# Optimization experiments

Hardware: AMD Instinct MI355X
Metric: run time of the kernel (lower is better)

Reference implementation:

```python
import jax, jax.numpy as jnp
import numpy as np

B, S, E, F = 8, 1024, 1024, 4096
EPS = 1e-12

def _layer_norm(x, gamma, beta):
    mu = jnp.mean(x, axis=-1, keepdims=True)
    var = jnp.mean(jnp.square(x - mu), axis=-1, keepdims=True)
    return (x - mu) / jnp.sqrt(var + EPS) * gamma + beta

def setup_inputs() -> dict:
    key = jax.random.key(0)
    ks = jax.random.split(key, 16)
    sE = 1.0 / np.sqrt(E)
    sF = 1.0 / np.sqrt(F)
    return {
        'hidden_states': jax.random.normal(ks[0], (B, S, E), jnp.float32),
        'Wq': jax.random.normal(ks[1], (E, E), jnp.float32) * sE,
        'bq': jnp.zeros((E,), jnp.float32),
        'Wk': jax.random.normal(ks[2], (E, E), jnp.float32) * sE,
        'bk': jnp.zeros((E,), jnp.float32),
        'Wv': jax.random.normal(ks[3], (E, E), jnp.float32) * sE,
        'bv': jnp.zeros((E,), jnp.float32),
        'Wd': jax.random.normal(ks[4], (E, E), jnp.float32) * sE,
        'bd': jnp.zeros((E,), jnp.float32),
        'g1': jnp.ones((E,), jnp.float32),
        'b1': jnp.zeros((E,), jnp.float32),
        'Wi': jax.random.normal(ks[5], (E, F), jnp.float32) * sE,
        'bi': jnp.zeros((F,), jnp.float32),
        'Wo': jax.random.normal(ks[6], (F, E), jnp.float32) * sF,
        'bo': jnp.zeros((E,), jnp.float32),
        'g2': jnp.ones((E,), jnp.float32),
        'b2': jnp.zeros((E,), jnp.float32),
    }

def reference(hidden_states, Wq, bq, Wk, bk, Wv, bv, Wd, bd, g1, b1, Wi, bi, Wo, bo, g2, b2):
    x = hidden_states
    q = x @ Wq + bq                     # [B,S,E]
    k = x @ Wk + bk
    v = x @ Wv + bv
    scores = jnp.einsum('bqe,bke->bqk', q, k) / jnp.sqrt(jnp.float32(E))
    attn_w = jax.nn.softmax(scores, axis=-1)
    attn_out = jnp.einsum('bqk,bke->bqe', attn_w, v)
    # add_norm 1 (dropout = identity in eval)
    h1 = _layer_norm(attn_out @ Wd + bd + x, g1, b1)
    ff = jax.nn.gelu(h1 @ Wi + bi, approximate=False)   # forward_act
    # NOTE: original code's second add_norm uses forward_act (pre out_dense),
    # applying out_dense inside add_norm -> LN(out_dense(ff) + h1)
    out = _layer_norm(ff @ Wo + bo + h1, g2, b2)
    return out
```

## Files before the change

kernel.cpp:

```cpp
#include <hip/hip_runtime.h>
#include <math.h>


typedef __bf16 bf16;
typedef __attribute__((ext_vector_type(8))) __bf16 bf16x8;
typedef __attribute__((ext_vector_type(4))) __bf16 bf16x4;
typedef __attribute__((ext_vector_type(4))) float f32x4;

#define BM 128
#define BN 128
#define BK 64
#define SCS 140

__device__ __forceinline__ void async_cp16(const bf16* g, bf16* l) {
    __builtin_amdgcn_global_load_lds((__attribute__((address_space(1))) void*)(g),
                                     (__attribute__((address_space(3))) void*)(l),
                                     16, 0, 0);
}

__device__ __forceinline__ float gelu_fast(float x) {
    float u = x * x;
    float y = 1.5957691216f * x * fmaf(0.044715f, u, 1.0f);
    float e = __expf(-y);
    return x * __builtin_amdgcn_rcpf(1.0f + e);
}

__device__ __forceinline__ float load_dual(const void* p, long long i, int f32) {
    return f32 ? ((const float*)p)[i] : (float)((const bf16*)p)[i];
}


__global__ void diag_init(const void* x, int* dflag)
{
    const int t = threadIdx.x;
    const bf16* xb = (const bf16*)x;
    float a = (float)xb[2 * t];
    float b = (float)xb[2 * t + 1];
    auto wild = [](float v) -> bool {
        float af = fabsf(v);
        return !(af <= 3.0e38f) || af > 1.0e3f || (v != 0.0f && af < 1.0e-8f);
    };
    unsigned long long ba = __ballot(wild(a));
    unsigned long long bb = __ballot(wild(b));
    if (t == 0) *dflag = (__popcll(ba) + __popcll(bb) > 16) ? 1 : 0;
}

__global__ void sentinel_small(float* out) { out[0] = 2048.0f; }


__global__ __launch_bounds__(256)
void convert_vec4(const void* src, bf16* dst, long long n4, const int* dflag)
{
    const int f32 = *dflag;
    long long i = (long long)blockIdx.x * 256 + threadIdx.x;
    if (i >= n4) return;
    bf16x4 o;
    if (f32) {
        f32x4 v = ((const f32x4*)src)[i];
        #pragma unroll
        for (int j = 0; j < 4; j++) o[j] = (bf16)v[j];
    } else {
        o = ((const bf16x4*)src)[i];
    }
    ((bf16x4*)dst)[i] = o;
}

struct SmallPtrs { const void* p[10]; };

__global__ __launch_bounds__(256)
void convert_small(SmallPtrs sp, bf16* dst, const int* dflag)
{
    const int f32 = *dflag;
    const int idx = blockIdx.x * 256 + threadIdx.x;
    if (idx >= 13312) return;
    const int seg = idx >> 10;
    float v;
    if (seg < 9) v = load_dual(sp.p[seg], idx & 1023, f32);
    else         v = load_dual(sp.p[9], idx - 9216, f32);
    dst[idx] = (bf16)v;
}

__global__ __launch_bounds__(256)
void transpose_dual(const void* in, bf16* out, int R, int C, const int* dflag)
{
    __shared__ bf16 tile[32][33];
    const int f32 = *dflag;
    const int c0 = blockIdx.x * 32, r0 = blockIdx.y * 32;
    const int tx = threadIdx.x, ty = threadIdx.y;
    #pragma unroll
    for (int i = 0; i < 32; i += 8)
        tile[ty + i][tx] = (bf16)load_dual(in, (long long)(r0 + ty + i) * C + (c0 + tx), f32);
    __syncthreads();
    #pragma unroll
    for (int i = 0; i < 32; i += 8)
        out[(long long)(c0 + ty + i) * R + (r0 + tx)] = tile[tx][ty + i];
}

__global__ __launch_bounds__(256)
void transpose_b(const bf16* __restrict__ in, bf16* __restrict__ out, int R, int C)
{
    __shared__ bf16 tile[32][33];
    const long long z = (long long)blockIdx.z * (long long)R * C;
    const int c0 = blockIdx.x * 32, r0 = blockIdx.y * 32;
    const int tx = threadIdx.x, ty = threadIdx.y;
    #pragma unroll
    for (int i = 0; i < 32; i += 8)
        tile[ty + i][tx] = in[z + (long long)(r0 + ty + i) * C + (c0 + tx)];
    __syncthreads();
    #pragma unroll
    for (int i = 0; i < 32; i += 8)
        out[z + (long long)(c0 + ty + i) * R + (r0 + tx)] = tile[tx][ty + i];
}

template<int ACT, int HAS_BIAS, int HAS_RES, int OUT_F32>
__global__ __launch_bounds__(512)
void gemm_bt(const bf16* __restrict__ A, const bf16* __restrict__ Bt,
             const bf16* __restrict__ bias, const bf16* __restrict__ res,
             void* __restrict__ Cout, int M, int N, int K, float scale,
             long long bsA, long long bsB, long long bsC, long long bsBias)
{
    __shared__ __align__(16) char smem[65536];
    float* sC = (float*)smem;

    const int tid  = threadIdx.x;
    const int lane = tid & 63;
    const int wave = tid >> 6;
    const int pw   = wave & 3;
    const int wm   = pw >> 1;
    const int wn   = pw & 1;
    const bool producer = (wave >= 4);
    const int m0   = blockIdx.y * BM;
    const int n0   = blockIdx.x * BN;
    const long long zA = (long long)blockIdx.z * bsA;
    const long long zB = (long long)blockIdx.z * bsB;
    const long long zC = (long long)blockIdx.z * bsC;
    const bf16* biasz = HAS_BIAS ? (bias + (long long)blockIdx.z * bsBias) : nullptr;
    const int nIter = K >> 6;

    f32x4 acc[4][4];
    const bf16* gA[4]; const bf16* gB[4]; int lo[4];

    if (producer) {
        #pragma unroll
        for (int j = 0; j < 4; j++) {
            const int ci  = j * 256 + pw * 64 + lane;
            const int row = ci >> 3;
            const int c8  = ((ci & 7) ^ (row & 7)) * 8;
            gA[j] = A + zA + (long long)(m0 + row) * K + c8;
            gB[j] = Bt + zB + (long long)(n0 + row) * K + c8;
            lo[j] = (j * 256 + pw * 64) * 8;
        }
        bf16* dA = (bf16*)smem;
        bf16* dB = (bf16*)(smem + 16384);
        #pragma unroll
        for (int j = 0; j < 4; j++) {
            async_cp16(gA[j], dA + lo[j]);
            async_cp16(gB[j], dB + lo[j]);
            gA[j] += BK; gB[j] += BK;
        }
    } else {
        const f32x4 zf = {0.f, 0.f, 0.f, 0.f};
        #pragma unroll
        for (int i = 0; i < 4; i++)
            #pragma unroll
            for (int j = 0; j < 4; j++) acc[i][j] = zf;
    }
    __syncthreads();

    const int fr   = lane & 15;
    const int x0   = (lane >> 4) ^ (fr & 7);
    const int arow = wm * 64 + fr;
    const int brow = wn * 64 + fr;

    for (int kt = 0; kt < nIter; ++kt) {
        if (producer) {
            if (kt + 1 < nIter) {
                const int bo = ((kt + 1) & 1) ? 32768 : 0;
                bf16* dA = (bf16*)(smem + bo);
                bf16* dB = (bf16*)(smem + bo + 16384);
                #pragma unroll
                for (int j = 0; j < 4; j++) {
                    async_cp16(gA[j], dA + lo[j]);
                    async_cp16(gB[j], dB + lo[j]);
                    gA[j] += BK; gB[j] += BK;
                }
            }
        } else {
            const int bo = (kt & 1) ? 32768 : 0;
            const bf16* sAk = (const bf16*)(smem + bo);
            const bf16* sBk = (const bf16*)(smem + bo + 16384);
            #pragma unroll
            for (int s = 0; s < 2; s++) {
                const int xo = (x0 ^ (s << 2)) * 8;
                bf16x8 afr[4], bfr[4];
                #pragma unroll
                for (int mi = 0; mi < 4; mi++) afr[mi] = *(const bf16x8*)(sAk + (arow + mi * 16) * 64 + xo);
                #pragma unroll
                for (int ni = 0; ni < 4; ni++) bfr[ni] = *(const bf16x8*)(sBk + (brow + ni * 16) * 64 + xo);
                #pragma unroll
                for (int mi = 0; mi < 4; mi++)
                    #pragma unroll
                    for (int ni = 0; ni < 4; ni++)
                        acc[mi][ni] = __builtin_amdgcn_mfma_f32_16x16x32_bf16(afr[mi], bfr[ni], acc[mi][ni], 0, 0, 0);
            }
        }
        __syncthreads();
    }

    const int q4 = lane >> 4;
    for (int h = 0; h < 2; h++) {
        __syncthreads();
        if (!producer && wm == h) {
            #pragma unroll
            for (int mi = 0; mi < 4; mi++)
                #pragma unroll
                for (int r = 0; r < 4; r++) {
                    const int lr = mi * 16 + q4 * 4 + r;
                    #pragma unroll
                    for (int ni = 0; ni < 4; ni++)
                        sC[lr * SCS + wn * 64 + ni * 16 + fr] = acc[mi][ni][r];
                }
        }
        __syncthreads();
        const int lr = tid >> 3;
        const int cb = (tid & 7) * 16;
        const long long grow  = m0 + h * 64 + lr;
        const long long gbase = zC + grow * (long long)N + (n0 + cb);
        const float* srow = sC + lr * SCS + cb;
        #pragma unroll
        for (int g = 0; g < 2; g++) {
            f32x4 v0 = *(const f32x4*)(srow + g * 8);
            f32x4 v1 = *(const f32x4*)(srow + g * 8 + 4);
            float vv[8] = {v0[0], v0[1], v0[2], v0[3], v1[0], v1[1], v1[2], v1[3]};
            if constexpr (HAS_BIAS) {
                bf16x8 bb = *(const bf16x8*)(biasz + n0 + cb + g * 8);
                #pragma unroll
                for (int j = 0; j < 8; j++) vv[j] = vv[j] * scale + (float)bb[j];
            } else {
                #pragma unroll
                for (int j = 0; j < 8; j++) vv[j] *= scale;
            }
            if constexpr (ACT == 1) {
                #pragma unroll
                for (int j = 0; j < 8; j++) vv[j] = gelu_fast(vv[j]);
            }
            if constexpr (HAS_RES) {
                bf16x8 rr = *(const bf16x8*)(res + gbase + g * 8);
                #pragma unroll
                for (int j = 0; j < 8; j++) vv[j] += (float)rr[j];
            }
            if constexpr (OUT_F32) {
                f32x4 o0 = {vv[0], vv[1], vv[2], vv[3]};
                f32x4 o1 = {vv[4], vv[5], vv[6], vv[7]};
                *(f32x4*)((float*)Cout + gbase + g * 8)     = o0;
                *(f32x4*)((float*)Cout + gbase + g * 8 + 4) = o1;
            } else {
                bf16x8 o;
                #pragma unroll
                for (int j = 0; j < 8; j++) o[j] = (bf16)vv[j];
                *(bf16x8*)((bf16*)Cout + gbase + g * 8) = o;
            }
        }
    }
}

template<int ACT, int HAS_BIAS, int HAS_RES, int OUT_F32, int SPLITK>
__global__ __launch_bounds__(512, 2)
void gemm256(const bf16* __restrict__ A, const bf16* __restrict__ Bt,
             const bf16* __restrict__ bias, const bf16* __restrict__ res,
             void* __restrict__ Cout, void* __restrict__ Cout2,
             int M, int N, int K, int ldk, float scale,
             long long bsB, long long bsC, long long bsBias)
{
    __shared__ __align__(16) char smem[131072];

    const int tid  = threadIdx.x;
    const int lane = tid & 63;
    const int wave = tid >> 6;
    const int wm   = wave >> 2;
    const int wn   = wave & 3;

    const int gx  = N >> 8;
    const int nwg = gx * (M >> 8);
    int wg = blockIdx.x;
    {
        const int q = nwg >> 3, r = nwg & 7;
        const int xcd = wg & 7, lid = wg >> 3;
        wg = (xcd < r ? xcd * (q + 1) : r * (q + 1) + (xcd - r) * q) + lid;
    }
    const int bx = wg % gx, by = wg / gx;
    const int m0 = by << 8, n0 = bx << 8;
    const int zi = blockIdx.y;

    const bf16* Ab = A  + (SPLITK ? (long long)zi * K : 0);
    const bf16* Bb = Bt + (SPLITK ? (long long)zi * K : (long long)zi * bsB);
    const bool  bon = HAS_BIAS && (!SPLITK || zi == 0);
    const bool  ron = HAS_RES  && (!SPLITK || zi == 0);
    const bf16* biasz = HAS_BIAS ? (bias + (SPLITK ? 0 : (long long)zi * bsBias)) : nullptr;
    const long long coff = SPLITK ? 0 : (long long)zi * bsC;
    char* const Cb = (char*)((SPLITK && zi) ? Cout2 : Cout);

    int soff[2];
    #pragma unroll
    for (int qq = 0; qq < 2; qq++) {
        const int g   = (wave * 2 + qq) * 64 + lane;
        const int rp  = g >> 3, sub = g & 7;
        const int row = rp * 2 + (sub >> 2);
        const int cc  = (sub & 3) ^ (rp & 3);
        soff[qq] = row * ldk + cc * 8;
    }
    const bf16* aS0 = Ab + (long long)m0 * ldk + soff[0];
    const bf16* aS1 = Ab + (long long)m0 * ldk + soff[1];
    const bf16* bS0 = Bb + (long long)n0 * ldk + soff[0];
    const bf16* bS1 = Bb + (long long)n0 * ldk + soff[1];
    char* const ldsW = smem + wave * 2048;

    const int fr = lane & 15, chk = lane >> 4;
    const int ra  = wm * 128 + fr;
    const int aRd = (ra >> 1) * 128 + (ra & 1) * 64 + ((chk ^ ((ra >> 1) & 3)) * 16);
    const int rb  = wn * 64 + fr;
    const int bRd = 32768 + (rb >> 1) * 128 + (rb & 1) * 64 + ((chk ^ ((rb >> 1) & 3)) * 16);

    unsigned aAddr[4], bAddr[4];
    {
        const unsigned sm3 = (unsigned)(size_t)(__attribute__((address_space(3))) char*)smem;
        #pragma unroll
        for (int cb = 0; cb < 2; cb++)
            #pragma unroll
            for (int s = 0; s < 2; s++) {
                aAddr[cb * 2 + s] = sm3 + cb * 65536 + s * 16384 + aRd;
                bAddr[cb * 2 + s] = sm3 + cb * 65536 + s * 16384 + bRd;
            }
    }

#define DSR(d, b, imm) \
    asm volatile("ds_read_b128 %0, %1 offset:%c2" : "=v"(d) : "v"(b), "i"(imm))

#define STG(buf, mat, h, t) do { \
    char* _d = ldsW + (buf) * 65536 + (mat) * 32768 + (h) * 16384; \
    const int _ko = (t) * 64 + (h) * 32; \
    async_cp16(((mat) ? bS0 : aS0) + _ko, (bf16*)_d); \
    async_cp16(((mat) ? bS1 : aS1) + _ko, (bf16*)(_d + 1024)); \
} while (0)
#define IF_STG(c, buf, mat, h, t) do { if (c) STG(buf, mat, h, t); } while (0)
#define NO_WAIT do {} while (0)
#define VM_WAIT(c) do { \
    if (c) asm volatile("s_waitcnt vmcnt(6)"); \
    else   asm volatile("s_waitcnt vmcnt(0)"); \
} while (0)
#define PHASE(cbuf, s, mh, DOB, STAGE_STMT, WAIT_STMT) do { \
    bf16x8 av0, av1, av2, av3; \
    DSR(av0, aAddr[(cbuf) * 2 + (s)], ((mh) * 4 + 0) * 1024); \
    DSR(av1, aAddr[(cbuf) * 2 + (s)], ((mh) * 4 + 1) * 1024); \
    DSR(av2, aAddr[(cbuf) * 2 + (s)], ((mh) * 4 + 2) * 1024); \
    DSR(av3, aAddr[(cbuf) * 2 + (s)], ((mh) * 4 + 3) * 1024); \
    if (DOB) { \
        DSR(bv[0], bAddr[(cbuf) * 2 + (s)], 0); \
        DSR(bv[1], bAddr[(cbuf) * 2 + (s)], 1024); \
        DSR(bv[2], bAddr[(cbuf) * 2 + (s)], 2048); \
        DSR(bv[3], bAddr[(cbuf) * 2 + (s)], 3072); \
    } \
    STAGE_STMT; \
    __builtin_amdgcn_s_barrier(); \
    asm volatile("s_waitcnt lgkmcnt(0)"); \
    __builtin_amdgcn_sched_barrier(0); \
    __builtin_amdgcn_s_setprio(1); \
    _Pragma("unroll") \
    for (int _j = 0; _j < 4; _j++) { \
        acc[(mh) * 4 + 0][_j] = __builtin_amdgcn_mfma_f32_16x16x32_bf16(av0, bv[_j], acc[(mh) * 4 + 0][_j], 0, 0, 0); \
        acc[(mh) * 4 + 1][_j] = __builtin_amdgcn_mfma_f32_16x16x32_bf16(av1, bv[_j], acc[(mh) * 4 + 1][_j], 0, 0, 0); \
        acc[(mh) * 4 + 2][_j] = __builtin_amdgcn_mfma_f32_16x16x32_bf16(av2, bv[_j], acc[(mh) * 4 + 2][_j], 0, 0, 0); \
        acc[(mh) * 4 + 3][_j] = __builtin_amdgcn_mfma_f32_16x16x32_bf16(av3, bv[_j], acc[(mh) * 4 + 3][_j], 0, 0, 0); \
    } \
    __builtin_amdgcn_s_setprio(0); \
    __builtin_amdgcn_sched_barrier(0); \
    WAIT_STMT; \
    __builtin_amdgcn_s_barrier(); \
} while (0)

    const int NT = K >> 6, NI = NT >> 1;

    STG(0, 1, 0, 0); STG(0, 0, 0, 0); STG(0, 1, 1, 0); STG(0, 0, 1, 0);
    STG(1, 1, 0, 1); STG(1, 0, 0, 1); STG(1, 1, 1, 1);

    f32x4 acc[8][4];
    {
        const f32x4 zf = {0.f, 0.f, 0.f, 0.f};
        #pragma unroll
        for (int i = 0; i < 8; i++)
            #pragma unroll
            for (int j = 0; j < 4; j++) acc[i][j] = zf;
    }
    bf16x8 bv[4];

    asm volatile("s_waitcnt vmcnt(6)");
    __builtin_amdgcn_s_barrier();

    for (int it = 0; it < NI; ++it) {
        const int o = 2 * it + 1, e2 = 2 * it + 2, o2 = 2 * it + 3;
        const bool se = e2 < NT, so = o2 < NT;
        PHASE(0, 0, 0, 1, STG(1, 0, 1, o),          NO_WAIT);
        PHASE(0, 0, 1, 0, IF_STG(se, 0, 1, 0, e2),  NO_WAIT);
        PHASE(0, 1, 0, 1, IF_STG(se, 0, 0, 0, e2),  NO_WAIT);
        PHASE(0, 1, 1, 0, IF_STG(se, 0, 1, 1, e2),  VM_WAIT(se));
        PHASE(1, 0, 0, 1, IF_STG(se, 0, 0, 1, e2),  NO_WAIT);
        PHASE(1, 0, 1, 0, IF_STG(so, 1, 1, 0, o2),  NO_WAIT);
        PHASE(1, 1, 0, 1, IF_STG(so, 1, 0, 0, o2),  NO_WAIT);
        PHASE(1, 1, 1, 0, IF_STG(so, 1, 1, 1, o2),  VM_WAIT(so));
    }
#undef PHASE
#undef VM_WAIT
#undef NO_WAIT
#undef IF_STG
#undef STG
#undef DSR

    float* sC = (float*)smem;
    const int q4 = lane >> 4;
    const int lr = tid >> 3;
    const int c0 = (tid & 7) * 4;
    const long long Nll = N;
    #pragma unroll
    for (int p = 0; p < 4; p++) {
        __syncthreads();
        if (wm == (p >> 1)) {
            #pragma unroll
            for (int i = 0; i < 4; i++) {
                const int fi = (p & 1) * 4 + i;
                #pragma unroll
                for (int r = 0; r < 4; r++) {
                    const int row = i * 16 + q4 * 4 + r;
                    #pragma unroll
                    for (int j = 0; j < 4; j++)
                        sC[row * 260 + wn * 64 + j * 16 + fr] = acc[fi][j][r];
                }
            }
        }
        __syncthreads();
        const long long grow = m0 + p * 64 + lr;
        const long long gb = grow * Nll + n0;
        const float* srow = sC + lr * 260;
        #pragma unroll
        for (int g = 0; g < 8; g++) {
            const int col = c0 + g * 32;
            f32x4 v = *(const f32x4*)(srow + col);
            float vv[4] = {v[0], v[1], v[2], v[3]};
            if (bon) {
                bf16x4 bb = *(const bf16x4*)(biasz + n0 + col);
                #pragma unroll
                for (int j = 0; j < 4; j++) vv[j] = vv[j] * scale + (float)bb[j];
            } else {
                #pragma unroll
                for (int j = 0; j < 4; j++) vv[j] *= scale;
            }
            if constexpr (ACT == 1) {
                #pragma unroll
                for (int j = 0; j < 4; j++) vv[j] = gelu_fast(vv[j]);
            }
            if (ron) {
                bf16x4 rr = *(const bf16x4*)(res + gb + col);
                #pragma unroll
                for (int j = 0; j < 4; j++) vv[j] += (float)rr[j];
            }
            if constexpr (OUT_F32) {
                f32x4 o4 = {vv[0], vv[1], vv[2], vv[3]};
                *(f32x4*)((float*)Cb + coff + gb + col) = o4;
            } else {
                bf16x4 o4;
                #pragma unroll
                for (int j = 0; j < 4; j++) o4[j] = (bf16)vv[j];
                *(bf16x4*)((bf16*)Cb + coff + gb + col) = o4;
            }
        }
    }
}


__global__ __launch_bounds__(256)
void softmax_inplace(bf16* __restrict__ P, int N)
{
    const long long row = blockIdx.x;
    bf16* p = P + row * (long long)N;
    const int t = threadIdx.x;
    bf16x4 xin = *(const bf16x4*)(p + t * 4);
    float xs[4];
    #pragma unroll
    for (int i = 0; i < 4; i++) xs[i] = (float)xin[i];

    float m = fmaxf(fmaxf(xs[0], xs[1]), fmaxf(xs[2], xs[3]));
    #pragma unroll
    for (int off = 32; off > 0; off >>= 1) m = fmaxf(m, __shfl_xor(m, off, 64));
    __shared__ float red[4];
    if ((t & 63) == 0) red[t >> 6] = m;
    __syncthreads();
    m = fmaxf(fmaxf(red[0], red[1]), fmaxf(red[2], red[3]));

    float e[4], s = 0.f;
    #pragma unroll
    for (int i = 0; i < 4; i++) { e[i] = __expf(xs[i] - m); s += e[i]; }
    #pragma unroll
    for (int off = 32; off > 0; off >>= 1) s += __shfl_xor(s, off, 64);
    __shared__ float red2[4];
    if ((t & 63) == 0) red2[t >> 6] = s;
    __syncthreads();
    s = red2[0] + red2[1] + red2[2] + red2[3];
    const float inv = 1.f / s;

    bf16x4 o;
    #pragma unroll
    for (int i = 0; i < 4; i++) o[i] = (bf16)(e[i] * inv);
    *(bf16x4*)(p + t * 4) = o;
}

template<int IN_MODE, int OUT_F32>
__global__ __launch_bounds__(256)
void layernorm_rows(const void* __restrict__ Z, const void* __restrict__ Z2,
                    const bf16* __restrict__ g, const bf16* __restrict__ b,
                    void* __restrict__ outp, int N)
{
    const long long row = blockIdx.x;
    const int t = threadIdx.x;
    float xv[4];
    if constexpr (IN_MODE >= 1) {
        f32x4 zin = *(const f32x4*)((const float*)Z + row * (long long)N + t * 4);
        #pragma unroll
        for (int i = 0; i < 4; i++) xv[i] = zin[i];
        if constexpr (IN_MODE == 2) {
            f32x4 z2 = *(const f32x4*)((const float*)Z2 + row * (long long)N + t * 4);
            #pragma unroll
            for (int i = 0; i < 4; i++) xv[i] += z2[i];
        }
    } else {
        bf16x4 zin = *(const bf16x4*)((const bf16*)Z + row * (long long)N + t * 4);
        #pragma unroll
        for (int i = 0; i < 4; i++) xv[i] = (float)zin[i];
    }

    float s = xv[0] + xv[1] + xv[2] + xv[3];
    #pragma unroll
    for (int off = 32; off > 0; off >>= 1) s += __shfl_xor(s, off, 64);
    __shared__ float r1[4];
    if ((t & 63) == 0) r1[t >> 6] = s;
    __syncthreads();
    const float mu = (r1[0] + r1[1] + r1[2] + r1[3]) * (1.f / 1024.f);

    float d[4];
    float sq = 0.f;
    #pragma unroll
    for (int i = 0; i < 4; i++) { d[i] = xv[i] - mu; sq += d[i] * d[i]; }
    #pragma unroll
    for (int off = 32; off > 0; off >>= 1) sq += __shfl_xor(sq, off, 64);
    __shared__ float r2[4];
    if ((t & 63) == 0) r2[t >> 6] = sq;
    __syncthreads();
    const float var = (r2[0] + r2[1] + r2[2] + r2[3]) * (1.f / 1024.f);
    const float rstd = rsqrtf(var + 1e-12f);

    bf16x4 gv = *(const bf16x4*)(g + t * 4);
    bf16x4 bv = *(const bf16x4*)(b + t * 4);
    if constexpr (OUT_F32) {
        f32x4 o;
        #pragma unroll
        for (int i = 0; i < 4; i++)
            o[i] = d[i] * rstd * (float)gv[i] + (float)bv[i];
        *(f32x4*)((float*)outp + row * (long long)N + t * 4) = o;
    } else {
        bf16x4 o;
        #pragma unroll
        for (int i = 0; i < 4; i++)
            o[i] = (bf16)(d[i] * rstd * (float)gv[i] + (float)bv[i]);
        *(bf16x4*)((bf16*)outp + row * (long long)N + t * 4) = o;
    }
}


extern "C" void kernel_launch(void* const* d_in, const int* in_sizes, int n_in,
                              void* d_out, int out_size, void* d_ws, size_t ws_size,
                              hipStream_t stream)
{
    (void)in_sizes; (void)n_in; (void)out_size;

    const void* x  = d_in[0];
    const void* Wq = d_in[1];  const void* bq = d_in[2];
    const void* Wk = d_in[3];  const void* bk = d_in[4];
    const void* Wv = d_in[5];  const void* bv = d_in[6];
    const void* Wd = d_in[7];  const void* bd = d_in[8];
    const void* g1 = d_in[9];  const void* b1 = d_in[10];
    const void* Wi = d_in[11]; const void* bi = d_in[12];
    const void* Wo = d_in[13]; const void* bo = d_in[14];
    const void* g2 = d_in[15]; const void* b2 = d_in[16];

    const int Bb = 8, S = 1024, E = 1024, F = 4096;
    const int M = Bb * S;
    const long long SE = (long long)S * E, SS = (long long)S * S;
    const long long ME = (long long)M * E;

    char* ws = (char*)d_ws;
    const size_t MB = 1024ull * 1024ull;
    int*  dflag = (int*)(ws + 0);
    bf16* small = (bf16*)(ws + 64 * 1024);
    bf16* bq_c = small + 0 * 1024;
    bf16* bd_c = small + 3 * 1024;
    bf16* g1_c = small + 4 * 1024;
    bf16* b1_c = small + 5 * 1024;
    bf16* g2_c = small + 6 * 1024;
    bf16* b2_c = small + 7 * 1024;
    bf16* bo_c = small + 8 * 1024;
    bf16* bi_c = small + 9216;
    bf16* WoT  = (bf16*)(ws + 1 * MB);
    bf16* WiT  = (bf16*)(ws + 9 * MB);
    bf16* WqT  = (bf16*)(ws + 17 * MB);
    bf16* WkT  = (bf16*)(ws + 19 * MB);
    bf16* WvT  = (bf16*)(ws + 21 * MB);
    bf16* WdT  = (bf16*)(ws + 23 * MB);
    bf16* xb   = (bf16*)(ws + 25 * MB);
    float* out = (float*)d_out;

    diag_init<<<1, 64, 0, stream>>>(x, dflag);

    if (ws_size < 70 * MB) { sentinel_small<<<1, 1, 0, stream>>>(out); return; }

    SmallPtrs sp;
    sp.p[0] = bq; sp.p[1] = bk; sp.p[2] = bv; sp.p[3] = bd; sp.p[4] = g1;
    sp.p[5] = b1; sp.p[6] = g2; sp.p[7] = b2; sp.p[8] = bo; sp.p[9] = bi;
    convert_small<<<52, 256, 0, stream>>>(sp, small, dflag);
    convert_vec4<<<8192, 256, 0, stream>>>(x, xb, ME / 4, dflag);

    const dim3 tb(32, 8, 1);
    transpose_dual<<<dim3(E/32, E/32), tb, 0, stream>>>(Wq, WqT, E, E, dflag);
    transpose_dual<<<dim3(E/32, E/32), tb, 0, stream>>>(Wk, WkT, E, E, dflag);
    transpose_dual<<<dim3(E/32, E/32), tb, 0, stream>>>(Wv, WvT, E, E, dflag);
    transpose_dual<<<dim3(E/32, E/32), tb, 0, stream>>>(Wd, WdT, E, E, dflag);
    transpose_dual<<<dim3(F/32, E/32), tb, 0, stream>>>(Wi, WiT, E, F, dflag);
    transpose_dual<<<dim3(E/32, F/32), tb, 0, stream>>>(Wo, WoT, F, E, dflag);

    if (ws_size >= 121 * MB) {
        bf16* qkv  = (bf16*)(ws + 41 * MB);
        bf16* q    = qkv;
        bf16* k    = qkv + ME;
        bf16* v    = qkv + 2 * ME;
        bf16* vT   = (bf16*)(ws + 89 * MB);
        bf16* P    = (bf16*)(ws + 73 * MB);
        bf16* attn = (bf16*)(ws + 41 * MB);
        bf16* z1   = (bf16*)(ws + 57 * MB);
        bf16* h1   = (bf16*)(ws + 41 * MB);
        bf16* ff   = (bf16*)(ws + 57 * MB);
        float* z2a = (float*)(ws + 9 * MB);
        float* z2b = (float*)(ws + 89 * MB);

        gemm256<0,1,0,0,0><<<dim3((E/256)*(M/256), 3), 512, 0, stream>>>(
            xb, WqT, bq_c, nullptr, qkv, nullptr, M, E, E, E, 1.f,
            (long long)E * E, ME, E);
        transpose_b<<<dim3(E/32, S/32, Bb), tb, 0, stream>>>(v, vT, S, E);
        gemm_bt<0,0,0,0><<<dim3(8, 8, Bb), 512, 0, stream>>>(
            q, k, nullptr, nullptr, P, S, S, E, 0.03125f, SE, SE, SS, 0);
        softmax_inplace<<<M, 256, 0, stream>>>(P, S);
        gemm_bt<0,0,0,0><<<dim3(8, 8, Bb), 512, 0, stream>>>(
            P, vT, nullptr, nullptr, attn, S, E, S, 1.f, SS, SE, SE, 0);
        gemm_bt<0,1,1,0><<<dim3(8, 64), 512, 0, stream>>>(
            attn, WdT, bd_c, xb, z1, M, E, E, 1.f, 0, 0, 0, 0);
        layernorm_rows<0,0><<<M, 256, 0, stream>>>(z1, nullptr, g1_c, b1_c, h1, E);
        gemm256<1,1,0,0,0><<<dim3((F/256)*(M/256), 1), 512, 0, stream>>>(
            h1, WiT, bi_c, nullptr, ff, nullptr, M, F, E, E, 1.f, 0, 0, 0);
        gemm256<0,1,1,1,1><<<dim3((E/256)*(M/256), 2), 512, 0, stream>>>(
            ff, WoT, bo_c, h1, z2a, z2b, M, E, F / 2, F, 1.f, 0, 0, 0);
        layernorm_rows<2,1><<<M, 256, 0, stream>>>(z2a, z2b, g2_c, b2_c, out, E);
    } else {
        bf16* qkv_b = (bf16*)(ws + 41 * MB);
        bf16* q_b   = qkv_b;
        bf16* k_b   = qkv_b + SE;
        bf16* v_b   = qkv_b + 2 * SE;
        bf16* vT_b  = (bf16*)(ws + 47 * MB);
        bf16* P_b   = (bf16*)(ws + 49 * MB);
        bf16* at_b  = (bf16*)(ws + 51 * MB);
        bf16* z1_b  = (bf16*)(ws + 53 * MB);
        bf16* h1_b  = (bf16*)(ws + 55 * MB);
        bf16* ff_b  = (bf16*)(ws + 57 * MB);
        bf16* z2_b  = (bf16*)(ws + 65 * MB);

        for (int b = 0; b < Bb; b++) {
            const bf16* x_b = xb + (long long)b * SE;
            gemm_bt<0,1,0,0><<<dim3(8, 8, 3), 512, 0, stream>>>(
                x_b, WqT, bq_c, nullptr, qkv_b, S, E, E, 1.f, 0, (long long)E * E, SE, E);
            transpose_b<<<dim3(E/32, S/32), tb, 0, stream>>>(v_b, vT_b, S, E);
            gemm_bt<0,0,0,0><<<dim3(8, 8), 512, 0, stream>>>(
                q_b, k_b, nullptr, nullptr, P_b, S, S, E, 0.03125f, 0, 0, 0, 0);
            softmax_inplace<<<S, 256, 0, stream>>>(P_b, S);
            gemm_bt<0,0,0,0><<<dim3(8, 8), 512, 0, stream>>>(
                P_b, vT_b, nullptr, nullptr, at_b, S, E, S, 1.f, 0, 0, 0, 0);
            gemm_bt<0,1,1,0><<<dim3(8, 8), 512, 0, stream>>>(
                at_b, WdT, bd_c, x_b, z1_b, S, E, E, 1.f, 0, 0, 0, 0);
            layernorm_rows<0,0><<<S, 256, 0, stream>>>(z1_b, nullptr, g1_c, b1_c, h1_b, E);
            gemm_bt<1,1,0,0><<<dim3(32, 8), 512, 0, stream>>>(
                h1_b, WiT, bi_c, nullptr, ff_b, S, F, E, 1.f, 0, 0, 0, 0);
            gemm_bt<0,1,1,0><<<dim3(8, 8), 512, 0, stream>>>(
                ff_b, WoT, bo_c, h1_b, z2_b, S, E, F, 1.f, 0, 0, 0, 0);
            layernorm_rows<0,1><<<S, 256, 0, stream>>>(z2_b, nullptr, g2_c, b2_c, out + (long long)b * SE, E);
        }
    }
}
```

Baseline: 517.9 us.

## Double-buffer MFMA operand registers to overlap LDS reads with matrix math

Restructures the GEMM main loop so the next phase's A/B fragments are read from LDS into a second register set while the current set feeds the MFMAs. This hides shared-memory read latency behind matrix core work instead of waiting on lgkmcnt before every compute phase. It costs extra VGPRs for the duplicated fragment sets, which may lower occupancy, and it adds more barriers per iteration.

```diff
diff --git a/kernel.cpp b/kernel.cpp
--- a/kernel.cpp
+++ b/kernel.cpp
@@ -335,7 +335,18 @@
 
 #define DSR(d, b, imm) \
     asm volatile("ds_read_b128 %0, %1 offset:%c2" : "=v"(d) : "v"(b), "i"(imm))
-
+#define RDA(set, idx, mh) do { \
+    DSR(set[0], aAddr[idx], ((mh) * 4 + 0) * 1024); \
+    DSR(set[1], aAddr[idx], ((mh) * 4 + 1) * 1024); \
+    DSR(set[2], aAddr[idx], ((mh) * 4 + 2) * 1024); \
+    DSR(set[3], aAddr[idx], ((mh) * 4 + 3) * 1024); \
+} while (0)
+#define RDB(set, idx) do { \
+    DSR(set[0], bAddr[idx], 0); \
+    DSR(set[1], bAddr[idx], 1024); \
+    DSR(set[2], bAddr[idx], 2048); \
+    DSR(set[3], bAddr[idx], 3072); \
+} while (0)
 #define STG(buf, mat, h, t) do { \
     char* _d = ldsW + (buf) * 65536 + (mat) * 32768 + (h) * 16384; \
     const int _ko = (t) * 64 + (h) * 32; \
@@ -343,39 +354,23 @@
     async_cp16(((mat) ? bS1 : aS1) + _ko, (bf16*)(_d + 1024)); \
 } while (0)
 #define IF_STG(c, buf, mat, h, t) do { if (c) STG(buf, mat, h, t); } while (0)
-#define NO_WAIT do {} while (0)
+#define BARR __builtin_amdgcn_s_barrier()
+#define SB0  __builtin_amdgcn_sched_barrier(0)
+#define LGKM0 asm volatile("s_waitcnt lgkmcnt(0)")
 #define VM_WAIT(c) do { \
     if (c) asm volatile("s_waitcnt vmcnt(6)"); \
     else   asm volatile("s_waitcnt vmcnt(0)"); \
 } while (0)
-#define PHASE(cbuf, s, mh, DOB, STAGE_STMT, WAIT_STMT) do { \
-    bf16x8 av0, av1, av2, av3; \
-    DSR(av0, aAddr[(cbuf) * 2 + (s)], ((mh) * 4 + 0) * 1024); \
-    DSR(av1, aAddr[(cbuf) * 2 + (s)], ((mh) * 4 + 1) * 1024); \
-    DSR(av2, aAddr[(cbuf) * 2 + (s)], ((mh) * 4 + 2) * 1024); \
-    DSR(av3, aAddr[(cbuf) * 2 + (s)], ((mh) * 4 + 3) * 1024); \
-    if (DOB) { \
-        DSR(bv[0], bAddr[(cbuf) * 2 + (s)], 0); \
-        DSR(bv[1], bAddr[(cbuf) * 2 + (s)], 1024); \
-        DSR(bv[2], bAddr[(cbuf) * 2 + (s)], 2048); \
-        DSR(bv[3], bAddr[(cbuf) * 2 + (s)], 3072); \
-    } \
-    STAGE_STMT; \
-    __builtin_amdgcn_s_barrier(); \
-    asm volatile("s_waitcnt lgkmcnt(0)"); \
-    __builtin_amdgcn_sched_barrier(0); \
+#define MMA(ASET, BSET, mh) do { \
     __builtin_amdgcn_s_setprio(1); \
     _Pragma("unroll") \
     for (int _j = 0; _j < 4; _j++) { \
-        acc[(mh) * 4 + 0][_j] = __builtin_amdgcn_mfma_f32_16x16x32_bf16(av0, bv[_j], acc[(mh) * 4 + 0][_j], 0, 0, 0); \
-        acc[(mh) * 4 + 1][_j] = __builtin_amdgcn_mfma_f32_16x16x32_bf16(av1, bv[_j], acc[(mh) * 4 + 1][_j], 0, 0, 0); \
-        acc[(mh) * 4 + 2][_j] = __builtin_amdgcn_mfma_f32_16x16x32_bf16(av2, bv[_j], acc[(mh) * 4 + 2][_j], 0, 0, 0); \
-        acc[(mh) * 4 + 3][_j] = __builtin_amdgcn_mfma_f32_16x16x32_bf16(av3, bv[_j], acc[(mh) * 4 + 3][_j], 0, 0, 0); \
+        acc[(mh) * 4 + 0][_j] = __builtin_amdgcn_mfma_f32_16x16x32_bf16(ASET[0], BSET[_j], acc[(mh) * 4 + 0][_j], 0, 0, 0); \
+        acc[(mh) * 4 + 1][_j] = __builtin_amdgcn_mfma_f32_16x16x32_bf16(ASET[1], BSET[_j], acc[(mh) * 4 + 1][_j], 0, 0, 0); \
+        acc[(mh) * 4 + 2][_j] = __builtin_amdgcn_mfma_f32_16x16x32_bf16(ASET[2], BSET[_j], acc[(mh) * 4 + 2][_j], 0, 0, 0); \
+        acc[(mh) * 4 + 3][_j] = __builtin_amdgcn_mfma_f32_16x16x32_bf16(ASET[3], BSET[_j], acc[(mh) * 4 + 3][_j], 0, 0, 0); \
     } \
     __builtin_amdgcn_s_setprio(0); \
-    __builtin_amdgcn_sched_barrier(0); \
-    WAIT_STMT; \
-    __builtin_amdgcn_s_barrier(); \
 } while (0)
 
     const int NT = K >> 6, NI = NT >> 1;
@@ -391,28 +386,74 @@
             #pragma unroll
             for (int j = 0; j < 4; j++) acc[i][j] = zf;
     }
-    bf16x8 bv[4];
+    bf16x8 avA[4], avB[4], bvA[4], bvB[4];
 
     asm volatile("s_waitcnt vmcnt(6)");
-    __builtin_amdgcn_s_barrier();
+    BARR;
 
     for (int it = 0; it < NI; ++it) {
         const int o = 2 * it + 1, e2 = 2 * it + 2, o2 = 2 * it + 3;
         const bool se = e2 < NT, so = o2 < NT;
-        PHASE(0, 0, 0, 1, STG(1, 0, 1, o),          NO_WAIT);
-        PHASE(0, 0, 1, 0, IF_STG(se, 0, 1, 0, e2),  NO_WAIT);
-        PHASE(0, 1, 0, 1, IF_STG(se, 0, 0, 0, e2),  NO_WAIT);
-        PHASE(0, 1, 1, 0, IF_STG(se, 0, 1, 1, e2),  VM_WAIT(se));
-        PHASE(1, 0, 0, 1, IF_STG(se, 0, 0, 1, e2),  NO_WAIT);
-        PHASE(1, 0, 1, 0, IF_STG(so, 1, 1, 0, o2),  NO_WAIT);
-        PHASE(1, 1, 0, 1, IF_STG(so, 1, 0, 0, o2),  NO_WAIT);
-        PHASE(1, 1, 1, 0, IF_STG(so, 1, 1, 1, o2),  VM_WAIT(so));
-    }
-#undef PHASE
+        RDA(avA, 0, 0); RDB(bvA, 0);
+        STG(1, 0, 1, o);
+        BARR; LGKM0; SB0;
+        RDA(avB, 0, 1);
+        SB0;
+        MMA(avA, bvA, 0);
+        BARR;
+        IF_STG(se, 0, 1, 0, e2);
+        BARR; LGKM0; SB0;
+        RDA(avA, 1, 0); RDB(bvB, 1);
+        SB0;
+        MMA(avB, bvA, 1);
+        BARR;
+        IF_STG(se, 0, 0, 0, e2);
+        BARR; LGKM0; SB0;
+        RDA(avB, 1, 1);
+        SB0;
+        MMA(avA, bvB, 0);
+        BARR;
+        IF_STG(se, 0, 1, 1, e2);
+        BARR; LGKM0; SB0;
+        MMA(avB, bvB, 1);
+        SB0;
+        VM_WAIT(se);
+        BARR;
+        RDA(avA, 2, 0); RDB(bvA, 2);
+        IF_STG(se, 0, 0, 1, e2);
+        BARR; LGKM0; SB0;
+        RDA(avB, 2, 1);
+        SB0;
+        MMA(avA, bvA, 0);
+        BARR;
+        IF_STG(so, 1, 1, 0, o2);
+        BARR; LGKM0; SB0;
+        RDA(avA, 3, 0); RDB(bvB, 3);
+        SB0;
+        MMA(avB, bvA, 1);
+        BARR;
+        IF_STG(so, 1, 0, 0, o2);
+        BARR; LGKM0; SB0;
+        RDA(avB, 3, 1);
+        SB0;
+        MMA(avA, bvB, 0);
+        BARR;
+        IF_STG(so, 1, 1, 1, o2);
+        BARR; LGKM0; SB0;
+        MMA(avB, bvB, 1);
+        SB0;
+        VM_WAIT(so);
+        BARR;
+    }
+#undef MMA
 #undef VM_WAIT
-#undef NO_WAIT
+#undef LGKM0
+#undef SB0
+#undef BARR
 #undef IF_STG
 #undef STG
+#undef RDB
+#undef RDA
 #undef DSR
 
     float* sC = (float*)smem;
```

Measured after the change: 507.5 us. 2.0% less time.

## Replace 256x256 GEMM with 128x128 double-buffered kernel for all GEMMs

Applied to the files above, without the earlier changes.

Replaces the 256x256 tile GEMM, with its 8-phase staged pipeline and 128KB LDS, by a 128x128 tile kernel. The new kernel uses a simple two-buffer ping-pong in 64KB LDS and allows 4 workgroups per CU. The same kernel now also runs the attention GEMMs and the Wd projection, which previously used gemm_bt, through a new per-batch A stride. The FFN output GEMM drops split-K and writes a single fp32 buffer. The aim is better occupancy and wave balance across CUs, at the cost of lower per-tile data reuse and a less finely overlapped load schedule.

```diff
diff --git a/kernel.cpp b/kernel.cpp
--- a/kernel.cpp
+++ b/kernel.cpp
@@ -265,14 +265,14 @@
 }
 
 template<int ACT, int HAS_BIAS, int HAS_RES, int OUT_F32, int SPLITK>
-__global__ __launch_bounds__(512, 2)
-void gemm256(const bf16* __restrict__ A, const bf16* __restrict__ Bt,
-             const bf16* __restrict__ bias, const bf16* __restrict__ res,
-             void* __restrict__ Cout, void* __restrict__ Cout2,
-             int M, int N, int K, int ldk, float scale,
-             long long bsB, long long bsC, long long bsBias)
-{
-    __shared__ __align__(16) char smem[131072];
+__global__ __launch_bounds__(512, 4)
+void gemm128d(const bf16* __restrict__ A, const bf16* __restrict__ Bt,
+              const bf16* __restrict__ bias, const bf16* __restrict__ res,
+              void* __restrict__ Cout, void* __restrict__ Cout2,
+              int M, int N, int K, int ldk, float scale,
+              long long bsA, long long bsB, long long bsC, long long bsBias)
+{
+    __shared__ __align__(16) char smem[65536];
 
     const int tid  = threadIdx.x;
     const int lane = tid & 63;
@@ -280,8 +280,8 @@
     const int wm   = wave >> 2;
     const int wn   = wave & 3;
 
-    const int gx  = N >> 8;
-    const int nwg = gx * (M >> 8);
+    const int gx  = N >> 7;
+    const int nwg = gx * (M >> 7);
     int wg = blockIdx.x;
     {
         const int q = nwg >> 3, r = nwg & 7;
@@ -289,10 +289,10 @@
         wg = (xcd < r ? xcd * (q + 1) : r * (q + 1) + (xcd - r) * q) + lid;
     }
     const int bx = wg % gx, by = wg / gx;
-    const int m0 = by << 8, n0 = bx << 8;
+    const int m0 = by << 7, n0 = bx << 7;
     const int zi = blockIdx.y;
 
-    const bf16* Ab = A  + (SPLITK ? (long long)zi * K : 0);
+    const bf16* Ab = A  + (SPLITK ? (long long)zi * K : (long long)zi * bsA);
     const bf16* Bb = Bt + (SPLITK ? (long long)zi * K : (long long)zi * bsB);
     const bool  bon = HAS_BIAS && (!SPLITK || zi == 0);
     const bool  ron = HAS_RES  && (!SPLITK || zi == 0);
@@ -300,119 +300,99 @@
     const long long coff = SPLITK ? 0 : (long long)zi * bsC;
     char* const Cb = (char*)((SPLITK && zi) ? Cout2 : Cout);
 
-    int soff[2];
-    #pragma unroll
-    for (int qq = 0; qq < 2; qq++) {
-        const int g   = (wave * 2 + qq) * 64 + lane;
-        const int rp  = g >> 3, sub = g & 7;
-        const int row = rp * 2 + (sub >> 2);
-        const int cc  = (sub & 3) ^ (rp & 3);
-        soff[qq] = row * ldk + cc * 8;
-    }
-    const bf16* aS0 = Ab + (long long)m0 * ldk + soff[0];
-    const bf16* aS1 = Ab + (long long)m0 * ldk + soff[1];
-    const bf16* bS0 = Bb + (long long)n0 * ldk + soff[0];
-    const bf16* bS1 = Bb + (long long)n0 * ldk + soff[1];
-    char* const ldsW = smem + wave * 2048;
+    const int rg0 = wave * 16 + (lane >> 3);
+    const int cg0 = (lane & 7) ^ (lane >> 3);
+    const bf16* aSrc = Ab + (long long)(m0 + rg0) * ldk + cg0 * 8;
+    const bf16* bSrc = Bb + (long long)(n0 + rg0) * ldk + cg0 * 8;
+    const int sq8 = 8 * ldk;
 
     const int fr = lane & 15, chk = lane >> 4;
-    const int ra  = wm * 128 + fr;
-    const int aRd = (ra >> 1) * 128 + (ra & 1) * 64 + ((chk ^ ((ra >> 1) & 3)) * 16);
-    const int rb  = wn * 64 + fr;
-    const int bRd = 32768 + (rb >> 1) * 128 + (rb & 1) * 64 + ((chk ^ ((rb >> 1) & 3)) * 16);
-
-    unsigned aAddr[4], bAddr[4];
+    unsigned aAd[2][2], bAd[2][2];
     {
         const unsigned sm3 = (unsigned)(size_t)(__attribute__((address_space(3))) char*)smem;
         #pragma unroll
-        for (int cb = 0; cb < 2; cb++)
+        for (int p = 0; p < 2; p++)
             #pragma unroll
-            for (int s = 0; s < 2; s++) {
-                aAddr[cb * 2 + s] = sm3 + cb * 65536 + s * 16384 + aRd;
-                bAddr[cb * 2 + s] = sm3 + cb * 65536 + s * 16384 + bRd;
+            for (int kk = 0; kk < 2; kk++) {
+                const unsigned slot = (unsigned)(((kk * 4 + chk) ^ (fr & 7)) * 16);
+                aAd[p][kk] = sm3 + p * 32768 + (wm * 64 + fr) * 128 + slot;
+                bAd[p][kk] = sm3 + p * 32768 + 16384 + (wn * 32 + fr) * 128 + slot;
             }
     }
 
 #define DSR(d, b, imm) \
     asm volatile("ds_read_b128 %0, %1 offset:%c2" : "=v"(d) : "v"(b), "i"(imm))
-
-#define STG(buf, mat, h, t) do { \
-    char* _d = ldsW + (buf) * 65536 + (mat) * 32768 + (h) * 16384; \
-    const int _ko = (t) * 64 + (h) * 32; \
-    async_cp16(((mat) ? bS0 : aS0) + _ko, (bf16*)_d); \
-    async_cp16(((mat) ? bS1 : aS1) + _ko, (bf16*)(_d + 1024)); \
+#define MM8(mh) do { \
+    _Pragma("unroll") \
+    for (int _n = 0; _n < 2; _n++) { \
+        acc[(mh) * 2 + 0][_n] = __builtin_amdgcn_mfma_f32_16x16x32_bf16(av[((mh) * 2 + 0) * 2 + 0], bv[_n * 2 + 0], acc[(mh) * 2 + 0][_n], 0, 0, 0); \
+        acc[(mh) * 2 + 1][_n] = __builtin_amdgcn_mfma_f32_16x16x32_bf16(av[((mh) * 2 + 1) * 2 + 0], bv[_n * 2 + 0], acc[(mh) * 2 + 1][_n], 0, 0, 0); \
+    } \
+    _Pragma("unroll") \
+    for (int _n = 0; _n < 2; _n++) { \
+        acc[(mh) * 2 + 0][_n] = __builtin_amdgcn_mfma_f32_16x16x32_bf16(av[((mh) * 2 + 0) * 2 + 1], bv[_n * 2 + 1], acc[(mh) * 2 + 0][_n], 0, 0, 0); \
+        acc[(mh) * 2 + 1][_n] = __builtin_amdgcn_mfma_f32_16x16x32_bf16(av[((mh) * 2 + 1) * 2 + 1], bv[_n * 2 + 1], acc[(mh) * 2 + 1][_n], 0, 0, 0); \
+    } \
 } while (0)
-#define IF_STG(c, buf, mat, h, t) do { if (c) STG(buf, mat, h, t); } while (0)
-#define NO_WAIT do {} while (0)
-#define VM_WAIT(c) do { \
-    if (c) asm volatile("s_waitcnt vmcnt(6)"); \
-    else   asm volatile("s_waitcnt vmcnt(0)"); \
-} while (0)
-#define PHASE(cbuf, s, mh, DOB, STAGE_STMT, WAIT_STMT) do { \
-    bf16x8 av0, av1, av2, av3; \
-    DSR(av0, aAddr[(cbuf) * 2 + (s)], ((mh) * 4 + 0) * 1024); \
-    DSR(av1, aAddr[(cbuf) * 2 + (s)], ((mh) * 4 + 1) * 1024); \
-    DSR(av2, aAddr[(cbuf) * 2 + (s)], ((mh) * 4 + 2) * 1024); \
-    DSR(av3, aAddr[(cbuf) * 2 + (s)], ((mh) * 4 + 3) * 1024); \
-    if (DOB) { \
-        DSR(bv[0], bAddr[(cbuf) * 2 + (s)], 0); \
-        DSR(bv[1], bAddr[(cbuf) * 2 + (s)], 1024); \
-        DSR(bv[2], bAddr[(cbuf) * 2 + (s)], 2048); \
-        DSR(bv[3], bAddr[(cbuf) * 2 + (s)], 3072); \
+#define TILE(p, SC) do { \
+    DSR(bv[0], bAd[p][0], 0);    DSR(bv[1], bAd[p][1], 0); \
+    DSR(bv[2], bAd[p][0], 2048); DSR(bv[3], bAd[p][1], 2048); \
+    DSR(av[0], aAd[p][0], 0);    DSR(av[1], aAd[p][1], 0); \
+    DSR(av[2], aAd[p][0], 2048); DSR(av[3], aAd[p][1], 2048); \
+    DSR(av[4], aAd[p][0], 4096); DSR(av[5], aAd[p][1], 4096); \
+    DSR(av[6], aAd[p][0], 6144); DSR(av[7], aAd[p][1], 6144); \
+    if (SC) { \
+        bf16* _dA = (bf16*)(smem + ((p) ^ 1) * 32768 + wave * 2048); \
+        bf16* _dB = (bf16*)(smem + ((p) ^ 1) * 32768 + 16384 + wave * 2048); \
+        async_cp16(aSrc, _dA);       async_cp16(aSrc + sq8, _dA + 512); \
+        async_cp16(bSrc, _dB);       async_cp16(bSrc + sq8, _dB + 512); \
+        aSrc += 64; bSrc += 64; \
     } \
-    STAGE_STMT; \
-    __builtin_amdgcn_s_barrier(); \
+    asm volatile("s_waitcnt lgkmcnt(4)"); \
+    __builtin_amdgcn_sched_barrier(0); \
+    __builtin_amdgcn_s_setprio(1); \
+    MM8(0); \
+    __builtin_amdgcn_s_setprio(0); \
     asm volatile("s_waitcnt lgkmcnt(0)"); \
     __builtin_amdgcn_sched_barrier(0); \
     __builtin_amdgcn_s_setprio(1); \
-    _Pragma("unroll") \
-    for (int _j = 0; _j < 4; _j++) { \
-        acc[(mh) * 4 + 0][_j] = __builtin_amdgcn_mfma_f32_16x16x32_bf16(av0, bv[_j], acc[(mh) * 4 + 0][_j], 0, 0, 0); \
-        acc[(mh) * 4 + 1][_j] = __builtin_amdgcn_mfma_f32_16x16x32_bf16(av1, bv[_j], acc[(mh) * 4 + 1][_j], 0, 0, 0); \
-        acc[(mh) * 4 + 2][_j] = __builtin_amdgcn_mfma_f32_16x16x32_bf16(av2, bv[_j], acc[(mh) * 4 + 2][_j], 0, 0, 0); \
-        acc[(mh) * 4 + 3][_j] = __builtin_amdgcn_mfma_f32_16x16x32_bf16(av3, bv[_j], acc[(mh) * 4 + 3][_j], 0, 0, 0); \
-    } \
+    MM8(1); \
     __builtin_amdgcn_s_setprio(0); \
     __builtin_amdgcn_sched_barrier(0); \
-    WAIT_STMT; \
+    asm volatile("s_waitcnt vmcnt(0)"); \
     __builtin_amdgcn_s_barrier(); \
 } while (0)
 
-    const int NT = K >> 6, NI = NT >> 1;
-
-    STG(0, 1, 0, 0); STG(0, 0, 0, 0); STG(0, 1, 1, 0); STG(0, 0, 1, 0);
-    STG(1, 1, 0, 1); STG(1, 0, 0, 1); STG(1, 1, 1, 1);
-
-    f32x4 acc[8][4];
+    const int NT = K >> 6, NH = NT >> 1;
+
+    {
+        bf16* dA = (bf16*)(smem + wave * 2048);
+        bf16* dB = (bf16*)(smem + 16384 + wave * 2048);
+        async_cp16(aSrc, dA);       async_cp16(aSrc + sq8, dA + 512);
+        async_cp16(bSrc, dB);       async_cp16(bSrc + sq8, dB + 512);
+        aSrc += 64; bSrc += 64;
+    }
+
+    f32x4 acc[4][2];
     {
         const f32x4 zf = {0.f, 0.f, 0.f, 0.f};
         #pragma unroll
-        for (int i = 0; i < 8; i++)
-            #pragma unroll
-            for (int j = 0; j < 4; j++) acc[i][j] = zf;
-    }
-    bf16x8 bv[4];
-
-    asm volatile("s_waitcnt vmcnt(6)");
+        for (int i = 0; i < 4; i++) {
+            acc[i][0] = zf; acc[i][1] = zf;
+        }
+    }
+    bf16x8 av[8], bv[4];
+
+    asm volatile("s_waitcnt vmcnt(0)");
     __builtin_amdgcn_s_barrier();
 
-    for (int it = 0; it < NI; ++it) {
-        const int o = 2 * it + 1, e2 = 2 * it + 2, o2 = 2 * it + 3;
-        const bool se = e2 < NT, so = o2 < NT;
-        PHASE(0, 0, 0, 1, STG(1, 0, 1, o),          NO_WAIT);
-        PHASE(0, 0, 1, 0, IF_STG(se, 0, 1, 0, e2),  NO_WAIT);
-        PHASE(0, 1, 0, 1, IF_STG(se, 0, 0, 0, e2),  NO_WAIT);
-        PHASE(0, 1, 1, 0, IF_STG(se, 0, 1, 1, e2),  VM_WAIT(se));
-        PHASE(1, 0, 0, 1, IF_STG(se, 0, 0, 1, e2),  NO_WAIT);
-        PHASE(1, 0, 1, 0, IF_STG(so, 1, 1, 0, o2),  NO_WAIT);
-        PHASE(1, 1, 0, 1, IF_STG(so, 1, 0, 0, o2),  NO_WAIT);
-        PHASE(1, 1, 1, 0, IF_STG(so, 1, 1, 1, o2),  VM_WAIT(so));
-    }
-#undef PHASE
-#undef VM_WAIT
-#undef NO_WAIT
-#undef IF_STG
-#undef STG
+    for (int it = 0; it < NH; ++it) {
+        const bool so = (it + 1 < NH);
+        TILE(0, true);
+        TILE(1, so);
+    }
+#undef TILE
+#undef MM8
 #undef DSR
 
     float* sC = (float*)smem;
@@ -421,27 +401,25 @@
     const int c0 = (tid & 7) * 4;
     const long long Nll = N;
     #pragma unroll
-    for (int p = 0; p < 4; p++) {
+    for (int p2 = 0; p2 < 2; p2++) {
         __syncthreads();
-        if (wm == (p >> 1)) {
+        if (wm == p2) {
             #pragma unroll
-            for (int i = 0; i < 4; i++) {
-                const int fi = (p & 1) * 4 + i;
+            for (int mi = 0; mi < 4; mi++)
                 #pragma unroll
                 for (int r = 0; r < 4; r++) {
-                    const int row = i * 16 + q4 * 4 + r;
+                    const int row = mi * 16 + q4 * 4 + r;
                     #pragma unroll
-                    for (int j = 0; j < 4; j++)
-                        sC[row * 260 + wn * 64 + j * 16 + fr] = acc[fi][j][r];
+                    for (int ni = 0; ni < 2; ni++)
+                        sC[row * 132 + wn * 32 + ni * 16 + fr] = acc[mi][ni][r];
                 }
-            }
         }
         __syncthreads();
-        const long long grow = m0 + p * 64 + lr;
+        const long long grow = m0 + p2 * 64 + lr;
         const long long gb = grow * Nll + n0;
-        const float* srow = sC + lr * 260;
-        #pragma unroll
-        for (int g = 0; g < 8; g++) {
+        const float* srow = sC + lr * 132;
+        #pragma unroll
+        for (int g = 0; g < 4; g++) {
             const int col = c0 + g * 32;
             f32x4 v = *(const f32x4*)(srow + col);
             float vv[4] = {v[0], v[1], v[2], v[3]};
@@ -645,26 +623,27 @@
         bf16* z1   = (bf16*)(ws + 57 * MB);
         bf16* h1   = (bf16*)(ws + 41 * MB);
         bf16* ff   = (bf16*)(ws + 57 * MB);
-        float* z2a = (float*)(ws + 9 * MB);
-        float* z2b = (float*)(ws + 89 * MB);
-
-        gemm256<0,1,0,0,0><<<dim3((E/256)*(M/256), 3), 512, 0, stream>>>(
+        float* z2f = (float*)(ws + 9 * MB);
+
+        gemm128d<0,1,0,0,0><<<dim3((E/128)*(M/128), 3), 512, 0, stream>>>(
             xb, WqT, bq_c, nullptr, qkv, nullptr, M, E, E, E, 1.f,
-            (long long)E * E, ME, E);
+            0, (long long)E * E, ME, E);
         transpose_b<<<dim3(E/32, S/32, Bb), tb, 0, stream>>>(v, vT, S, E);
-        gemm_bt<0,0,0,0><<<dim3(8, 8, Bb), 512, 0, stream>>>(
-            q, k, nullptr, nullptr, P, S, S, E, 0.03125f, SE, SE, SS, 0);
+        gemm128d<0,0,0,0,0><<<dim3((S/128)*(S/128), Bb), 512, 0, stream>>>(
+            q, k, nullptr, nullptr, P, nullptr, S, S, E, E, 0.03125f,
+            SE, SE, SS, 0);
         softmax_inplace<<<M, 256, 0, stream>>>(P, S);
-        gemm_bt<0,0,0,0><<<dim3(8, 8, Bb), 512, 0, stream>>>(
-            P, vT, nullptr, nullptr, attn, S, E, S, 1.f, SS, SE, SE, 0);
-        gemm_bt<0,1,1,0><<<dim3(8, 64), 512, 0, stream>>>(
-            attn, WdT, bd_c, xb, z1, M, E, E, 1.f, 0, 0, 0, 0);
+        gemm128d<0,0,0,0,0><<<dim3((E/128)*(S/128), Bb), 512, 0, stream>>>(
+            P, vT, nullptr, nullptr, attn, nullptr, S, E, S, S, 1.f,
+            SS, SE, SE, 0);
+        gemm128d<0,1,1,0,0><<<dim3((E/128)*(M/128), 1), 512, 0, stream>>>(
+            attn, WdT, bd_c, xb, z1, nullptr, M, E, E, E, 1.f, 0, 0, 0, 0);
         layernorm_rows<0,0><<<M, 256, 0, stream>>>(z1, nullptr, g1_c, b1_c, h1, E);
-        gemm256<1,1,0,0,0><<<dim3((F/256)*(M/256), 1), 512, 0, stream>>>(
-            h1, WiT, bi_c, nullptr, ff, nullptr, M, F, E, E, 1.f, 0, 0, 0);
-        gemm256<0,1,1,1,1><<<dim3((E/256)*(M/256), 2), 512, 0, stream>>>(
-            ff, WoT, bo_c, h1, z2a, z2b, M, E, F / 2, F, 1.f, 0, 0, 0);
-        layernorm_rows<2,1><<<M, 256, 0, stream>>>(z2a, z2b, g2_c, b2_c, out, E);
+        gemm128d<1,1,0,0,0><<<dim3((F/128)*(M/128), 1), 512, 0, stream>>>(
+            h1, WiT, bi_c, nullptr, ff, nullptr, M, F, E, E, 1.f, 0, 0, 0, 0);
+        gemm128d<0,1,1,1,0><<<dim3((E/128)*(M/128), 1), 512, 0, stream>>>(
+            ff, WoT, bo_c, h1, z2f, nullptr, M, E, F, F, 1.f, 0, 0, 0, 0);
+        layernorm_rows<1,1><<<M, 256, 0, stream>>>(z2f, nullptr, g2_c, b2_c, out, E);
     } else {
         bf16* qkv_b = (bf16*)(ws + 41 * MB);
         bf16* q_b   = qkv_b;
```

After: 472.1 us. 8.8% less time.
